# Kernel optimization log

Measured on AMD Instinct MI355X. Metric: run time of the kernel, lower is better.

## Reference

```python
import jax, jax.numpy as jnp
import numpy as np

N = 100000       # nodes
E = 1000000      # edges
NFEAT = 128
NHID = 256
NCLASS = 40
THRESHOLD = 0.1
EPS = 1e-8


def setup_inputs() -> dict:
    key = jax.random.key(0)
    k = jax.random.split(key, 5)
    x = jax.random.normal(k[0], (N, NFEAT), dtype=jnp.float32)
    row = jax.random.randint(k[1], (E,), 0, N)
    col = jax.random.randint(k[2], (E,), 0, N)
    W1 = jax.random.normal(k[3], (NFEAT, NHID), dtype=jnp.float32) / np.sqrt(NFEAT).astype(np.float32)
    b1 = jnp.zeros((NHID,), jnp.float32)
    W2 = jax.random.normal(k[4], (NHID, NCLASS), dtype=jnp.float32) / np.sqrt(NHID).astype(np.float32)
    b2 = jnp.zeros((NCLASS,), jnp.float32)
    return {"x": x, "row": row, "col": col, "W1": W1, "b1": b1, "W2": W2, "b2": b2}


def _att_coef(feat, row, col, prev_mask=None):
    # per-edge cosine similarity (F.cosine_similarity semantics, eps=1e-8)
    nrm = jnp.maximum(jnp.linalg.norm(feat, axis=1), EPS)  # [N]
    dots = jnp.sum(feat[row] * feat[col], axis=1)          # [E] gather-heavy
    sims = dots / (nrm[row] * nrm[col])
    mask = (sims >= THRESHOLD) & (row != col)
    if prev_mask is not None:
        # edges dropped by a previous att_coef no longer exist in the adj
        mask = mask & prev_mask
    # torch.no_grad in original -> weights are constants
    w = jax.lax.stop_gradient(jnp.where(mask, sims, 0.0))
    return w, mask


def _gcn_conv(x, row, col, w, W, b):
    # PyG GCNConv(add_self_loops=True, normalize=True) with edge weights w.
    # Zero-weight edges are exactly equivalent to removed edges.
    h = x @ W                                             # [N, out]
    deg = jnp.zeros((N,), h.dtype).at[row].add(w) + 1.0   # + self-loop weight 1
    dinv = jax.lax.rsqrt(deg)
    norm = dinv[row] * w * dinv[col]                      # [E]
    out = jnp.zeros((N, h.shape[1]), h.dtype).at[row].add(norm[:, None] * h[col])
    out = out + (dinv * dinv)[:, None] * h                # self-loop contribution
    return out + b


def reference(x, row, col, W1, b1, W2, b2):
    w1, m1 = _att_coef(x, row, col)
    h = _gcn_conv(x, row, col, w1, W1, b1)
    h = jax.nn.relu(h)
    # dropout in eval mode -> identity
    w2, _ = _att_coef(h, row, col, prev_mask=m1)
    out = _gcn_conv(h, row, col, w2, W2, b2)
    return out
```

## Files before the change

### kernel.cpp

```cpp
#include <hip/hip_runtime.h>
#include <hip/hip_bf16.h>
#include <hip/hip_fp16.h>

#define NFEAT 128
#define NHID  256
#define NCLASS 40
#define THRESH 0.1f
#define FEPS   1e-8f
#define GUARD2 4e-3f
#define NSTRIPE 384

typedef _Float16 v2h __attribute__((ext_vector_type(2)));
typedef _Float16 v8h __attribute__((ext_vector_type(8)));
typedef float f32x4 __attribute__((ext_vector_type(4)));

__device__ __forceinline__ float dot2acc(unsigned int a, unsigned int b, float s) {
#if __has_builtin(__builtin_amdgcn_fdot2)
    return __builtin_amdgcn_fdot2(__builtin_bit_cast(v2h, a),
                                  __builtin_bit_cast(v2h, b), s, false);
#else
    float2 fa = __half22float2(__builtin_bit_cast(__half2, a));
    float2 fb = __half22float2(__builtin_bit_cast(__half2, b));
    return s + fa.x * fb.x + fa.y * fb.y;
#endif
}

__device__ __forceinline__ int dot4acc(int a, int b, int acc) {
#if __has_builtin(__builtin_amdgcn_sdot4)
    return __builtin_amdgcn_sdot4(a, b, acc, false);
#else
#pragma unroll
    for (int k = 0; k < 4; ++k) {
        int av = (a << (24 - 8 * k)) >> 24;
        int bv = (b << (24 - 8 * k)) >> 24;
        acc += av * bv;
    }
    return acc;
#endif
}

__device__ __forceinline__ float waveSum(float v) {
#pragma unroll
    for (int off = 32; off > 0; off >>= 1) v += __shfl_xor(v, off, 64);
    return v;
}

__device__ __forceinline__ float waveMax(float v) {
#pragma unroll
    for (int off = 32; off > 0; off >>= 1) v = fmaxf(v, __shfl_xor(v, off, 64));
    return v;
}

__global__ void k_prepw(const float* __restrict__ x,
                        signed char* __restrict__ xqi,
                        float4* __restrict__ meta,
                        float* __restrict__ nrm, float* __restrict__ deg,
                        float* __restrict__ deg2,
                        int* __restrict__ counts, float* __restrict__ nrmsq,
                        const float* __restrict__ W1f, v8h* __restrict__ w1x,
                        const float* __restrict__ W2f, v8h* __restrict__ w2x,
                        int N, int prepBlocks) {
    int b = blockIdx.x;
    int tid = threadIdx.x;
    if (b < prepBlocks) {
        int r = (b * 256 + tid) >> 6;
        int lane = tid & 63;
        if (r >= N) return;
        float2 a = ((const float2*)(x + (size_t)r * NFEAT))[lane];
        float s = waveSum(a.x * a.x + a.y * a.y);
        float nr = fmaxf(sqrtf(s), FEPS);
        float inv = 1.0f / nr;
        float xn0 = a.x * inv, xn1 = a.y * inv;
        float m = waveMax(fmaxf(fabsf(xn0), fabsf(xn1)));
        float t = (m > 0.f) ? 127.f / m : 0.f;
        float sc = m * (1.0f / 127.f);
        int q0 = __float2int_rn(xn0 * t), q1 = __float2int_rn(xn1 * t);
        q0 = max(-127, min(127, q0));
        q1 = max(-127, min(127, q1));
        char2 pk; pk.x = (signed char)q0; pk.y = (signed char)q1;
        ((char2*)(xqi + (size_t)r * 256))[lane] = pk;
        float rq = (m > 0.f) ? 256.0f / sc : 0.f;
        int l0 = __float2int_rn((xn0 - sc * (float)q0) * rq);
        int l1 = __float2int_rn((xn1 - sc * (float)q1) * rq);
        l0 = max(-128, min(127, l0));
        l1 = max(-128, min(127, l1));
        char2 pl; pl.x = (signed char)l0; pl.y = (signed char)l1;
        ((char2*)(xqi + (size_t)r * 256 + 128))[lane] = pl;
        float asum = waveSum((float)(abs(q0) + abs(q1)));
        float axn  = waveSum(fabsf(xn0) + fabsf(xn1));
        if (lane == 0) {
            meta[r] = make_float4(sc, 0.5f * asum + 33.0f, axn, 0.0f);
            nrm[r] = nr;
            deg[r] = 0.0f;
            deg2[r] = 0.0f;
            counts[r] = 0;
            nrmsq[r] = 0.0f;
        }
    } else if (b < prepBlocks + 16) {
        int id = (b - prepBlocks) * 256 + tid;
        int frag = id >> 6, lane = id & 63;
        int kb = frag >> 4, ct = frag & 15;
        int kbase = kb * 32 + (lane >> 4) * 8;
        int n = ct * 16 + (lane & 15);
        v8h v;
#pragma unroll
        for (int j = 0; j < 8; ++j)
            v[j] = (_Float16)W1f[(size_t)(kbase + j) * NHID + n];
        w1x[id] = v;
    } else {
        int id = (b - prepBlocks - 16) * 256 + tid;
        int part = (id >= 1536) ? 1 : 0;
        int fid = id - part * 1536;
        int frag = fid >> 6, lane = fid & 63;
        int kb = frag / 3, ct = frag % 3;
        int kbase = kb * 32 + (lane >> 4) * 8;
        int n = ct * 16 + (lane & 15);
        v8h v;
#pragma unroll
        for (int j = 0; j < 8; ++j) {
            float wv = (n < NCLASS) ? W2f[(size_t)(kbase + j) * NCLASS + n] : 0.0f;
            _Float16 hi = (_Float16)wv;
            v[j] = part ? (_Float16)(wv - (float)hi) : hi;
        }
        w2x[id] = v;
    }
}

__global__ void k_att1(const float* __restrict__ xf,
                       const signed char* __restrict__ xqi,
                       const float4* __restrict__ meta,
                       const int* __restrict__ row, const int* __restrict__ col,
                       const float* __restrict__ nrm,
                       float* __restrict__ w1, float* __restrict__ deg,
                       int* __restrict__ counts, int E) {
    int wid = (blockIdx.x * blockDim.x + threadIdx.x) >> 6;
    int lane = threadIdx.x & 63;
    int l4 = lane & 3;
    int e = wid * 16 + (lane >> 2);
    if (e >= E) return;
    int r = row[e], c = col[e];
    const int4* qra = (const int4*)(xqi + (size_t)r * 256);
    const int4* qca = (const int4*)(xqi + (size_t)c * 256);
    int4 qa0 = qra[l4 * 2], qa1 = qra[l4 * 2 + 1];
    int4 qb0 = qca[l4 * 2], qb1 = qca[l4 * 2 + 1];
    int d = 0;
    d = dot4acc(qa0.x, qb0.x, d); d = dot4acc(qa0.y, qb0.y, d);
    d = dot4acc(qa0.z, qb0.z, d); d = dot4acc(qa0.w, qb0.w, d);
    d = dot4acc(qa1.x, qb1.x, d); d = dot4acc(qa1.y, qb1.y, d);
    d = dot4acc(qa1.z, qb1.z, d); d = dot4acc(qa1.w, qb1.w, d);
    d += __shfl_xor(d, 1, 64);
    d += __shfl_xor(d, 2, 64);
    float4 mr = meta[r], mc = meta[c];
    float ub = mr.x * mc.x * ((float)d + mr.y + mc.y);
    float sims = 0.0f;
    bool alive = (ub >= THRESH - 1e-5f);
    if (alive) {
        const int4* lra = (const int4*)(xqi + (size_t)r * 256 + 128);
        const int4* lca = (const int4*)(xqi + (size_t)c * 256 + 128);
        int4 la0 = lra[l4 * 2], la1 = lra[l4 * 2 + 1];
        int4 lb0 = lca[l4 * 2], lb1 = lca[l4 * 2 + 1];
        int dll = 0, dx = 0;
        dll = dot4acc(la0.x, lb0.x, dll); dll = dot4acc(la0.y, lb0.y, dll);
        dll = dot4acc(la0.z, lb0.z, dll); dll = dot4acc(la0.w, lb0.w, dll);
        dll = dot4acc(la1.x, lb1.x, dll); dll = dot4acc(la1.y, lb1.y, dll);
        dll = dot4acc(la1.z, lb1.z, dll); dll = dot4acc(la1.w, lb1.w, dll);
        dx = dot4acc(qa0.x, lb0.x, dx); dx = dot4acc(qa0.y, lb0.y, dx);
        dx = dot4acc(qa0.z, lb0.z, dx); dx = dot4acc(qa0.w, lb0.w, dx);
        dx = dot4acc(qa1.x, lb1.x, dx); dx = dot4acc(qa1.y, lb1.y, dx);
        dx = dot4acc(qa1.z, lb1.z, dx); dx = dot4acc(qa1.w, lb1.w, dx);
        dx = dot4acc(la0.x, qb0.x, dx); dx = dot4acc(la0.y, qb0.y, dx);
        dx = dot4acc(la0.z, qb0.z, dx); dx = dot4acc(la0.w, qb0.w, dx);
        dx = dot4acc(la1.x, qb1.x, dx); dx = dot4acc(la1.y, qb1.y, dx);
        dx = dot4acc(la1.z, qb1.z, dx); dx = dot4acc(la1.w, qb1.w, dx);
        int conf = dx * 256 + dll;
        conf += __shfl_xor(conf, 1, 64);
        conf += __shfl_xor(conf, 2, 64);
        float ss = mr.x * mc.x;
        sims = ss * ((float)d + (float)conf * (1.0f / 65536.f));
        float errB = (mr.x * mc.z + mc.x * mr.z) * (1.0f / 256.f) + ss * 0.01f + 2e-5f;
        if (__builtin_expect(fabsf(sims - THRESH) < errB, 0)) {
            const float4* fr = (const float4*)(xf + (size_t)r * NFEAT);
            const float4* fc = (const float4*)(xf + (size_t)c * NFEAT);
            float s2 = 0.f;
#pragma unroll
            for (int j = 0; j < 8; ++j) {
                float4 av = fr[l4 + 4 * j], bv = fc[l4 + 4 * j];
                s2 += av.x * bv.x + av.y * bv.y + av.z * bv.z + av.w * bv.w;
            }
            s2 += __shfl_xor(s2, 1, 64);
            s2 += __shfl_xor(s2, 2, 64);
            sims = s2 / (nrm[r] * nrm[c]);
        }
    }
    if (l4 == 0) {
        float w = (alive && sims >= THRESH && r != c) ? sims : 0.0f;
        w1[e] = w;
        if (w != 0.0f) {
            unsafeAtomicAdd(&deg[r], w);
            atomicAdd(&counts[r], 1);
        }
    }
}

__global__ __launch_bounds__(256) void k_scan1(const int* __restrict__ counts,
                                               int* __restrict__ rowptr,
                                               int* __restrict__ bsum, int N) {
    __shared__ int tmp[256];
    int t = threadIdx.x, i = blockIdx.x * 256 + t;
    int v = (i < N) ? counts[i] : 0;
    tmp[t] = v;
    __syncthreads();
    for (int off = 1; off < 256; off <<= 1) {
        int add = (t >= off) ? tmp[t - off] : 0;
        __syncthreads();
        tmp[t] += add;
        __syncthreads();
    }
    if (i < N) rowptr[i] = tmp[t] - v;
    if (t == 255) bsum[blockIdx.x] = tmp[t];
}

__global__ __launch_bounds__(512) void k_scan2(int* __restrict__ bsum, int nb) {
    __shared__ int tmp[512];
    int t = threadIdx.x;
    int v = (t < nb) ? bsum[t] : 0;
    tmp[t] = v;
    __syncthreads();
    for (int off = 1; off < 512; off <<= 1) {
        int add = (t >= off) ? tmp[t - off] : 0;
        __syncthreads();
        tmp[t] += add;
        __syncthreads();
    }
    if (t < nb) bsum[t] = tmp[t] - v;
}

__global__ void k_fill(const int* __restrict__ row, const int* __restrict__ col,
                       const float* __restrict__ wbuf, const float* __restrict__ deg,
                       int* __restrict__ rowptr, const int* __restrict__ bsum,
                       int2* __restrict__ edata, int* __restrict__ esrc, int E) {
    int e = blockIdx.x * blockDim.x + threadIdx.x;
    if (e >= E) return;
    float w = wbuf[e];
    if (w == 0.0f) return;
    int r = row[e], c = col[e];
    float dr = 1.0f / sqrtf(1.0f + deg[r]);
    float dc = 1.0f / sqrtf(1.0f + deg[c]);
    float nm = dr * w * dc;
    int pos = atomicAdd(&rowptr[r], 1) + bsum[r >> 8];
    edata[pos] = make_int2(c, __float_as_int(nm));
    esrc[pos] = r;
}

__global__ void k_gather1(const float* __restrict__ xf, const int* __restrict__ rowptr,
                          const int* __restrict__ bsum,
                          const int* __restrict__ counts, const float* __restrict__ deg,
                          const int2* __restrict__ edata, float* __restrict__ xagg, int N) {
    int tid = blockIdx.x * blockDim.x + threadIdx.x;
    int r = tid >> 3;
    int l = tid & 7;
    if (r >= N) return;
    int cnt = counts[r];
    int start = rowptr[r] + bsum[r >> 8] - cnt;
    float d = 1.0f / sqrtf(1.0f + deg[r]);
    float dd = d * d;
    const float4* xr = (const float4*)(xf + (size_t)r * NFEAT) + l * 4;
    float4 c0, c1, c2, c3;
    {
        float4 a0 = xr[0], a1 = xr[1], a2 = xr[2], a3 = xr[3];
        c0 = make_float4(dd * a0.x, dd * a0.y, dd * a0.z, dd * a0.w);
        c1 = make_float4(dd * a1.x, dd * a1.y, dd * a1.z, dd * a1.w);
        c2 = make_float4(dd * a2.x, dd * a2.y, dd * a2.z, dd * a2.w);
        c3 = make_float4(dd * a3.x, dd * a3.y, dd * a3.z, dd * a3.w);
    }
    for (int k = 0; k < cnt; ++k) {
        int2 ed = edata[start + k];
        float nm = __int_as_float(ed.y);
        const float4* xc = (const float4*)(xf + (size_t)ed.x * NFEAT) + l * 4;
        float4 b0 = xc[0], b1 = xc[1], b2 = xc[2], b3 = xc[3];
        c0.x += nm * b0.x; c0.y += nm * b0.y; c0.z += nm * b0.z; c0.w += nm * b0.w;
        c1.x += nm * b1.x; c1.y += nm * b1.y; c1.z += nm * b1.z; c1.w += nm * b1.w;
        c2.x += nm * b2.x; c2.y += nm * b2.y; c2.z += nm * b2.z; c2.w += nm * b2.w;
        c3.x += nm * b3.x; c3.y += nm * b3.y; c3.z += nm * b3.z; c3.w += nm * b3.w;
    }
    float4* xo = (float4*)(xagg + (size_t)r * NFEAT) + l * 4;
    xo[0] = c0; xo[1] = c1; xo[2] = c2; xo[3] = c3;
}

__global__ __launch_bounds__(256) void k_gemm1h(const float* __restrict__ xagg,
                                                const v8h* __restrict__ w1x,
                                                const float* __restrict__ b1f,
                                                __half* __restrict__ hh16,
                                                float* __restrict__ nrmsq, int N) {
    __shared__ __half2 xsh[64][68];
    __shared__ v8h bsh[4][8][64];
    int tid = threadIdx.x;
    int ch = blockIdx.x & 1;
    int stripe = blockIdx.x >> 1;

#pragma unroll
    for (int it = 0; it < 8; ++it) {
        int id = it * 256 + tid;
        int lane = id & 63, fr = id >> 6;
        int kb = fr >> 3, ctl = fr & 7;
        bsh[kb][ctl][lane] = w1x[(size_t)(kb * 16 + ch * 8 + ctl) * 64 + lane];
    }

    int w = tid >> 6, lane = tid & 63;
    int c = lane & 15, q = lane >> 4;
    int nb = w * 16;

    int T = (N + 63) >> 6;
    for (int t = stripe; t < T; t += NSTRIPE) {
        int i0 = t * 64;
        __syncthreads();

#pragma unroll
        for (int it = 0; it < 16; ++it) {
            int idx = it * 256 + tid;
            int n = idx >> 6, kq = idx & 63;
            int i = i0 + n;
            float2 v = make_float2(0.f, 0.f);
            if (i < N) v = ((const float2*)(xagg + (size_t)i * NFEAT))[kq];
            xsh[n][kq] = __floats2half2_rn(v.x, v.y);
        }
        __syncthreads();

        f32x4 acc[8];
#pragma unroll
        for (int ct = 0; ct < 8; ++ct) acc[ct] = (f32x4){0.f, 0.f, 0.f, 0.f};

#pragma unroll
        for (int kb = 0; kb < 4; ++kb) {
            v8h a = *((const v8h*)&xsh[nb + c][kb * 16 + q * 4]);
#pragma unroll
            for (int ctl = 0; ctl < 8; ++ctl) {
                acc[ctl] = __builtin_amdgcn_mfma_f32_16x16x32_f16(
                    a, bsh[kb][ctl][lane], acc[ctl], 0, 0, 0);
            }
        }

        float s2[4] = {0.f, 0.f, 0.f, 0.f};
        bool full = (i0 + 64 <= N);
#pragma unroll
        for (int ctl = 0; ctl < 8; ++ctl) {
            int n = (ch * 8 + ctl) * 16 + c;
            float bias = b1f[n];
            f32x4 d = acc[ctl];
#pragma unroll
            for (int reg = 0; reg < 4; ++reg) {
                int node = i0 + nb + q * 4 + reg;
                float v = fmaxf(d[reg] + bias, 0.f);
                s2[reg] += v * v;
                if (full || node < N) hh16[(size_t)node * NHID + n] = __float2half(v);
            }
        }
#pragma unroll
        for (int off = 1; off < 16; off <<= 1) {
#pragma unroll
            for (int reg = 0; reg < 4; ++reg) s2[reg] += __shfl_xor(s2[reg], off, 64);
        }
        if (c == 0) {
            int base = i0 + nb + q * 4;
#pragma unroll
            for (int reg = 0; reg < 4; ++reg)
                if (base + reg < N) unsafeAtomicAdd(&nrmsq[base + reg], s2[reg]);
        }
    }
}

__global__ __launch_bounds__(256) void k_l2fused(
        const __half2* __restrict__ hh, const v8h* __restrict__ w2x,
        float* __restrict__ g,
        const float* __restrict__ xagg, const float* __restrict__ W1f,
        const float* __restrict__ b1f, const int* __restrict__ esrc,
        const int2* __restrict__ edata, const float* __restrict__ nrmsq,
        const int* __restrict__ etot, const int* __restrict__ ebs,
        float* __restrict__ w2csr, float* __restrict__ deg2,
        int gemmBlocks, int N) {
    __shared__ __half2 hs[64][NHID / 2 + 4];
    int tid = threadIdx.x;
    if ((int)blockIdx.x < gemmBlocks) {
        int i0 = blockIdx.x * 64;
#pragma unroll
        for (int it = 0; it < 8; ++it) {
            int idx = it * 256 + tid;
            int n = idx >> 5, kq = idx & 31;
            int i = i0 + n;
            uint4 v = make_uint4(0u, 0u, 0u, 0u);
            if (i < N) v = ((const uint4*)(hh + (size_t)i * (NHID / 2)))[kq];
            *((uint4*)&hs[n][kq * 4]) = v;
        }
        __syncthreads();

        int w = tid >> 6, lane = tid & 63;
        int c = lane & 15, q = lane >> 4;
        int nb = w * 16;

        f32x4 acc[3];
#pragma unroll
        for (int t = 0; t < 3; ++t) acc[t] = (f32x4){0.f, 0.f, 0.f, 0.f};

#pragma unroll
        for (int kb = 0; kb < 8; ++kb) {
            v8h a = *((const v8h*)&hs[nb + c][kb * 16 + q * 4]);
            const v8h* bh = w2x + (size_t)(kb * 3) * 64 + lane;
            const v8h* bl = bh + 1536;
#pragma unroll
            for (int ct = 0; ct < 3; ++ct) {
                acc[ct] = __builtin_amdgcn_mfma_f32_16x16x32_f16(a, bh[ct * 64], acc[ct], 0, 0, 0);
                acc[ct] = __builtin_amdgcn_mfma_f32_16x16x32_f16(a, bl[ct * 64], acc[ct], 0, 0, 0);
            }
        }

        bool full = (i0 + 64 <= N);
#pragma unroll
        for (int ct = 0; ct < 3; ++ct) {
            int cls = ct * 16 + c;
            if (cls < NCLASS) {
                f32x4 d = acc[ct];
#pragma unroll
                for (int reg = 0; reg < 4; ++reg) {
                    int node = i0 + nb + q * 4 + reg;
                    if (full || node < N) g[(size_t)node * NCLASS + cls] = d[reg];
                }
            }
        }
    } else {
        int lane = tid & 63;
        int l8 = lane & 7, gr8 = lane >> 3;
        int nb2 = gridDim.x - gemmBlocks;
        int wid0 = (((int)blockIdx.x - gemmBlocks) * 256 + tid) >> 6;
        int step = (nb2 * 256) >> 3;
        int total = *etot + *ebs;
        for (int base = wid0 * 8; base < total; base += step) {
            int pos = base + gr8;
            bool active = (pos < total);
            int r = 0, c = 0;
            float sims = 0.f, inv = 0.f;
            if (active) {
                r = esrc[pos];
                c = edata[pos].x;
                const uint4* hr4 = (const uint4*)(hh + (size_t)r * (NHID / 2));
                const uint4* hc4 = (const uint4*)(hh + (size_t)c * (NHID / 2));
                float s = 0.f;
#pragma unroll
                for (int j = 0; j < 4; ++j) {
                    uint4 a = hr4[l8 + 8 * j];
                    uint4 b = hc4[l8 + 8 * j];
                    s = dot2acc(a.x, b.x, s); s = dot2acc(a.y, b.y, s);
                    s = dot2acc(a.z, b.z, s); s = dot2acc(a.w, b.w, s);
                }
                s += __shfl_xor(s, 1, 64);
                s += __shfl_xor(s, 2, 64);
                s += __shfl_xor(s, 4, 64);
                float nr = fmaxf(sqrtf(nrmsq[r]), FEPS);
                float nc = fmaxf(sqrtf(nrmsq[c]), FEPS);
                inv = 1.0f / (nr * nc);
                sims = s * inv;
            }
            unsigned long long gm =
                __ballot(active && l8 == 0 && fabsf(sims - THRESH) < GUARD2);
            while (gm) {
                int src = __ffsll(gm) - 1;
                gm &= gm - 1;
                int rr = __shfl(r, src, 64);
                int cc = __shfl(c, src, 64);
                float invv = __shfl(inv, src, 64);
                int j0 = lane * 4;
                float aR[4], aC[4];
#pragma unroll
                for (int q = 0; q < 4; ++q) { aR[q] = b1f[j0 + q]; aC[q] = b1f[j0 + q]; }
                const float* xr = xagg + (size_t)rr * NFEAT;
                const float* xc = xagg + (size_t)cc * NFEAT;
                for (int kk = 0; kk < NFEAT; ++kk) {
                    float vr = xr[kk], vc = xc[kk];
                    float4 wv = *((const float4*)(W1f + (size_t)kk * NHID + j0));
                    aR[0] += vr * wv.x; aC[0] += vc * wv.x;
                    aR[1] += vr * wv.y; aC[1] += vc * wv.y;
                    aR[2] += vr * wv.z; aC[2] += vc * wv.z;
                    aR[3] += vr * wv.w; aC[3] += vc * wv.w;
                }
                float dp = 0.f;
#pragma unroll
                for (int q = 0; q < 4; ++q)
                    dp += fmaxf(aR[q], 0.f) * fmaxf(aC[q], 0.f);
                float se = waveSum(dp) * invv;
                if (lane == src) sims = se;
            }
            if (active && l8 == 0) {
                float w2 = (sims >= THRESH) ? sims : 0.f;
                w2csr[pos] = w2;
                if (w2 != 0.f) unsafeAtomicAdd(&deg2[r], w2);
            }
        }
    }
}

__global__ void k_gather2(const float* __restrict__ g, const int* __restrict__ rowptr,
                          const int* __restrict__ bsum,
                          const int* __restrict__ counts, const float* __restrict__ deg2,
                          const float* __restrict__ b2f, const int2* __restrict__ edata,
                          const float* __restrict__ w2csr, float* __restrict__ out, int N) {
    int tid = blockIdx.x * blockDim.x + threadIdx.x;
    int r = tid >> 3;
    int l = tid & 7;
    if (r >= N) return;
    int cnt = counts[r];
    int start = rowptr[r] + bsum[r >> 8] - cnt;
    float dr = 1.0f / sqrtf(1.0f + deg2[r]);
    float drr = dr * dr;
    const float* gr = g + (size_t)r * NCLASS;
    float acc[5];
#pragma unroll
    for (int q = 0; q < 5; ++q) acc[q] = drr * gr[l + 8 * q] + b2f[l + 8 * q];
    for (int k = 0; k < cnt; ++k) {
        int2 ed = edata[start + k];
        float w2 = w2csr[start + k];
        float dc = 1.0f / sqrtf(1.0f + deg2[ed.x]);
        float f = dr * w2 * dc;
        const float* gc = g + (size_t)ed.x * NCLASS;
#pragma unroll
        for (int q = 0; q < 5; ++q) acc[q] += f * gc[l + 8 * q];
    }
    float* po = out + (size_t)r * NCLASS;
#pragma unroll
    for (int q = 0; q < 5; ++q) po[l + 8 * q] = acc[q];
}

extern "C" void kernel_launch(void* const* d_in, const int* in_sizes, int n_in,
                              void* d_out, int out_size, void* d_ws, size_t ws_size,
                              hipStream_t stream) {
    const float* x  = (const float*)d_in[0];
    const int* row  = (const int*)d_in[1];
    const int* col  = (const int*)d_in[2];
    const float* W1 = (const float*)d_in[3];
    const float* b1 = (const float*)d_in[4];
    const float* W2 = (const float*)d_in[5];
    const float* b2 = (const float*)d_in[6];
    float* out = (float*)d_out;
    const int N = in_sizes[0] / NFEAT;
    const int E = in_sizes[1];

    char* ws = (char*)d_ws;
    size_t off = 0;
    auto alloc = [&](size_t bytes) {
        char* p = ws + off;
        off += (bytes + 255) & ~(size_t)255;
        return p;
    };
    float*   xagg   = (float*)alloc((size_t)N * NFEAT * 4);
    __half2* hh     = (__half2*)alloc((size_t)N * NHID * 2);
    float*   w1buf  = (float*)alloc((size_t)E * 4);
    float*   w2csr  = (float*)alloc((size_t)E * 4);
    int2*    edata  = (int2*)alloc((size_t)E * 8);
    int*     esrc   = (int*)alloc((size_t)E * 4);
    float*   nrm    = (float*)alloc((size_t)N * 4);
    float*   deg    = (float*)alloc((size_t)N * 4);
    int*     counts = (int*)alloc((size_t)N * 4);
    int*     rowptr = (int*)alloc((size_t)N * 4);
    int*     bsum   = (int*)alloc(512 * 4);
    v8h*     w1x    = (v8h*)alloc(4096 * 16);
    v8h*     w2x    = (v8h*)alloc(3072 * 16);
    float*   nrmsq  = (float*)alloc((size_t)N * 4);
    float*   deg2   = (float*)alloc((size_t)N * 4);
    signed char* xqi = (signed char*)xagg;
    float4*  meta    = (float4*)(xqi + (size_t)N * 256);
    size_t gBytes = ((size_t)N * NCLASS * 4 + 255) & ~(size_t)255;
    bool fused = (off + gBytes <= ws_size);
    float* g = fused ? (float*)alloc(gBytes) : xagg;

    const int e16Blocks = (E + 63) / 64;
    const int eBlocks1 = (E + 255) / 256;
    const int nBlocks4 = (N + 3) / 4;
    const int nBlocks8 = (N + 31) / 32;
    const int scanB    = (N + 255) / 256;
    const int gemmB    = (N + 63) / 64;

    k_prepw<<<nBlocks4 + 28, 256, 0, stream>>>(x, xqi, meta, nrm, deg, deg2,
                                               counts, nrmsq, W1, w1x, W2, w2x,
                                               N, nBlocks4);
    k_att1<<<e16Blocks, 256, 0, stream>>>(x, xqi, meta, row, col, nrm, w1buf, deg,
                                          counts, E);
    k_scan1<<<scanB, 256, 0, stream>>>(counts, rowptr, bsum, N);
    k_scan2<<<1, 512, 0, stream>>>(bsum, scanB);
    k_fill<<<eBlocks1, 256, 0, stream>>>(row, col, w1buf, deg, rowptr, bsum, edata,
                                         esrc, E);
    k_gather1<<<nBlocks8, 256, 0, stream>>>(x, rowptr, bsum, counts, deg, edata,
                                            xagg, N);
    k_gemm1h<<<2 * NSTRIPE, 256, 0, stream>>>(xagg, w1x, b1, (__half*)hh, nrmsq, N);

    k_l2fused<<<gemmB + 4096, 256, 0, stream>>>(hh, w2x, g, xagg, W1, b1, esrc,
                                                edata, nrmsq, rowptr + (N - 1),
                                                bsum + ((N - 1) >> 8),
                                                w2csr, deg2, gemmB, N);
    k_gather2<<<nBlocks8, 256, 0, stream>>>(g, rowptr, bsum, counts, deg2, b2, edata,
                                            w2csr, out, N);
}
```

Baseline: 302.5 us.

## Emit fp16 aggregated features from gather and compute both column halves per GEMM block

The gather kernel now also writes a half-precision copy of the aggregated features, and the first GEMM reads that copy instead of converting fp32 to fp16 itself. Each GEMM block now handles both 128-column halves of its 64-row tile, reloading the W1 fragment into shared memory for each half, and the grid shrinks to NSTRIPE blocks. The aim is to halve the GEMM's input read traffic and stop two blocks from re-reading the same xagg tile. In exchange gather1 writes an extra buffer, the GEMM gets an extra barrier and reloads weights every tile, and fewer blocks run concurrently.

Result: faster. 296.3 us (-2.0%).

```diff
diff --git a/kernel.cpp b/kernel.cpp
--- a/kernel.cpp
+++ b/kernel.cpp
@@ -255,7 +255,8 @@
 __global__ void k_gather1(const float* __restrict__ xf, const int* __restrict__ rowptr,
                           const int* __restrict__ bsum,
                           const int* __restrict__ counts, const float* __restrict__ deg,
-                          const int2* __restrict__ edata, float* __restrict__ xagg, int N) {
+                          const int2* __restrict__ edata, float* __restrict__ xagg,
+                          __half2* __restrict__ xaggh, int N) {
     int tid = blockIdx.x * blockDim.x + threadIdx.x;
     int r = tid >> 3;
     int l = tid & 7;
@@ -285,9 +286,21 @@
     }
     float4* xo = (float4*)(xagg + (size_t)r * NFEAT) + l * 4;
     xo[0] = c0; xo[1] = c1; xo[2] = c2; xo[3] = c3;
-}
-
-__global__ __launch_bounds__(256) void k_gemm1h(const float* __restrict__ xagg,
+    union { uint4 u; __half2 h[4]; } p0, p1;
+    p0.h[0] = __floats2half2_rn(c0.x, c0.y);
+    p0.h[1] = __floats2half2_rn(c0.z, c0.w);
+    p0.h[2] = __floats2half2_rn(c1.x, c1.y);
+    p0.h[3] = __floats2half2_rn(c1.z, c1.w);
+    p1.h[0] = __floats2half2_rn(c2.x, c2.y);
+    p1.h[1] = __floats2half2_rn(c2.z, c2.w);
+    p1.h[2] = __floats2half2_rn(c3.x, c3.y);
+    p1.h[3] = __floats2half2_rn(c3.z, c3.w);
+    uint4* ho = (uint4*)(xaggh + (size_t)r * (NFEAT / 2));
+    ho[l * 2] = p0.u;
+    ho[l * 2 + 1] = p1.u;
+}
+
+__global__ __launch_bounds__(256) void k_gemm1h(const __half2* __restrict__ xaggh,
                                                 const v8h* __restrict__ w1x,
                                                 const float* __restrict__ b1f,
                                                 __half* __restrict__ hh16,
@@ -295,76 +308,77 @@
     __shared__ __half2 xsh[64][68];
     __shared__ v8h bsh[4][8][64];
     int tid = threadIdx.x;
-    int ch = blockIdx.x & 1;
-    int stripe = blockIdx.x >> 1;
-
-#pragma unroll
-    for (int it = 0; it < 8; ++it) {
-        int id = it * 256 + tid;
-        int lane = id & 63, fr = id >> 6;
-        int kb = fr >> 3, ctl = fr & 7;
-        bsh[kb][ctl][lane] = w1x[(size_t)(kb * 16 + ch * 8 + ctl) * 64 + lane];
-    }
-
     int w = tid >> 6, lane = tid & 63;
     int c = lane & 15, q = lane >> 4;
     int nb = w * 16;
 
     int T = (N + 63) >> 6;
-    for (int t = stripe; t < T; t += NSTRIPE) {
+    for (int t = blockIdx.x; t < T; t += NSTRIPE) {
         int i0 = t * 64;
         __syncthreads();
 
 #pragma unroll
-        for (int it = 0; it < 16; ++it) {
+        for (int it = 0; it < 4; ++it) {
             int idx = it * 256 + tid;
-            int n = idx >> 6, kq = idx & 63;
+            int n = idx >> 4, kq = idx & 15;
             int i = i0 + n;
-            float2 v = make_float2(0.f, 0.f);
-            if (i < N) v = ((const float2*)(xagg + (size_t)i * NFEAT))[kq];
-            xsh[n][kq] = __floats2half2_rn(v.x, v.y);
-        }
-        __syncthreads();
-
-        f32x4 acc[8];
-#pragma unroll
-        for (int ct = 0; ct < 8; ++ct) acc[ct] = (f32x4){0.f, 0.f, 0.f, 0.f};
-
-#pragma unroll
-        for (int kb = 0; kb < 4; ++kb) {
-            v8h a = *((const v8h*)&xsh[nb + c][kb * 16 + q * 4]);
+            uint4 v = make_uint4(0u, 0u, 0u, 0u);
+            if (i < N) v = ((const uint4*)(xaggh + (size_t)i * (NFEAT / 2)))[kq];
+            *((uint4*)&xsh[n][kq * 4]) = v;
+        }
+
+#pragma unroll
+        for (int ch = 0; ch < 2; ++ch) {
+            if (ch == 1) __syncthreads();
+#pragma unroll
+            for (int it = 0; it < 8; ++it) {
+                int id = it * 256 + tid;
+                int lane2 = id & 63, fr = id >> 6;
+                int kb = fr >> 3, ctl = fr & 7;
+                bsh[kb][ctl][lane2] = w1x[(size_t)(kb * 16 + ch * 8 + ctl) * 64 + lane2];
+            }
+            __syncthreads();
+
+            f32x4 acc[8];
+#pragma unroll
+            for (int ct = 0; ct < 8; ++ct) acc[ct] = (f32x4){0.f, 0.f, 0.f, 0.f};
+
+#pragma unroll
+            for (int kb = 0; kb < 4; ++kb) {
+                v8h a = *((const v8h*)&xsh[nb + c][kb * 16 + q * 4]);
+#pragma unroll
+                for (int ctl = 0; ctl < 8; ++ctl) {
+                    acc[ctl] = __builtin_amdgcn_mfma_f32_16x16x32_f16(
+                        a, bsh[kb][ctl][lane], acc[ctl], 0, 0, 0);
+                }
+            }
+
+            float s2[4] = {0.f, 0.f, 0.f, 0.f};
+            bool full = (i0 + 64 <= N);
 #pragma unroll
             for (int ctl = 0; ctl < 8; ++ctl) {
-                acc[ctl] = __builtin_amdgcn_mfma_f32_16x16x32_f16(
-                    a, bsh[kb][ctl][lane], acc[ctl], 0, 0, 0);
-            }
-        }
-
-        float s2[4] = {0.f, 0.f, 0.f, 0.f};
-        bool full = (i0 + 64 <= N);
-#pragma unroll
-        for (int ctl = 0; ctl < 8; ++ctl) {
-            int n = (ch * 8 + ctl) * 16 + c;
-            float bias = b1f[n];
-            f32x4 d = acc[ctl];
-#pragma unroll
-            for (int reg = 0; reg < 4; ++reg) {
-                int node = i0 + nb + q * 4 + reg;
-                float v = fmaxf(d[reg] + bias, 0.f);
-                s2[reg] += v * v;
-                if (full || node < N) hh16[(size_t)node * NHID + n] = __float2half(v);
-            }
-        }
-#pragma unroll
-        for (int off = 1; off < 16; off <<= 1) {
-#pragma unroll
-            for (int reg = 0; reg < 4; ++reg) s2[reg] += __shfl_xor(s2[reg], off, 64);
-        }
-        if (c == 0) {
-            int base = i0 + nb + q * 4;
-#pragma unroll
-            for (int reg = 0; reg < 4; ++reg)
-                if (base + reg < N) unsafeAtomicAdd(&nrmsq[base + reg], s2[reg]);
+                int n = (ch * 8 + ctl) * 16 + c;
+                float bias = b1f[n];
+                f32x4 dv = acc[ctl];
+#pragma unroll
+                for (int reg = 0; reg < 4; ++reg) {
+                    int node = i0 + nb + q * 4 + reg;
+                    float v = fmaxf(dv[reg] + bias, 0.f);
+                    s2[reg] += v * v;
+                    if (full || node < N) hh16[(size_t)node * NHID + n] = __float2half(v);
+                }
+            }
+#pragma unroll
+            for (int off = 1; off < 16; off <<= 1) {
+#pragma unroll
+                for (int reg = 0; reg < 4; ++reg) s2[reg] += __shfl_xor(s2[reg], off, 64);
+            }
+            if (c == 0) {
+                int base = i0 + nb + q * 4;
+#pragma unroll
+                for (int reg = 0; reg < 4; ++reg)
+                    if (base + reg < N) unsafeAtomicAdd(&nrmsq[base + reg], s2[reg]);
+            }
         }
     }
 }
@@ -551,6 +565,7 @@
     };
     float*   xagg   = (float*)alloc((size_t)N * NFEAT * 4);
     __half2* hh     = (__half2*)alloc((size_t)N * NHID * 2);
+    __half2* xaggh  = (__half2*)alloc((size_t)N * NFEAT * 2);
     float*   w1buf  = (float*)alloc((size_t)E * 4);
     float*   w2csr  = (float*)alloc((size_t)E * 4);
     int2*    edata  = (int2*)alloc((size_t)E * 8);
@@ -587,8 +602,8 @@
     k_fill<<<eBlocks1, 256, 0, stream>>>(row, col, w1buf, deg, rowptr, bsum, edata,
                                          esrc, E);
     k_gather1<<<nBlocks8, 256, 0, stream>>>(x, rowptr, bsum, counts, deg, edata,
-                                            xagg, N);
-    k_gemm1h<<<2 * NSTRIPE, 256, 0, stream>>>(xagg, w1x, b1, (__half*)hh, nrmsq, N);
+                                            xagg, xaggh, N);
+    k_gemm1h<<<NSTRIPE, 256, 0, stream>>>(xaggh, w1x, b1, (__half*)hh, nrmsq, N);
 
     k_l2fused<<<gemmB + 4096, 256, 0, stream>>>(hh, w2x, g, xagg, W1, b1, esrc,
                                                 edata, nrmsq, rowptr + (N - 1),
```
